# Kernel tuning notes

Hardware: AMD Instinct MI355X
Metric: run time of the kernel (lower is better)

Reference implementation:

```python
import jax, jax.numpy as jnp
import numpy as np

E = 256      # embed_dim
K = 8        # kNN neighbors (hard-coded in module)
B = 64       # num cells (samples)
P = 512      # objects per cell (equal segments)
N = B * P
NUM_CLASSES = 31  # 30 known + <unk> (padding idx 0)


def _normalize(x, axis=-1):
    n = jnp.linalg.norm(x, axis=axis, keepdims=True)
    return x / jnp.clip(n, 1e-12, None)


def _mlp2(x, W1, b1, W2, b2):
    # get_mlp([d_in, 64/E, d_out]): Linear-ReLU-Linear
    return jax.nn.relu(x @ W1 + b1) @ W2 + b2


def setup_inputs() -> dict:
    key = jax.random.key(0)
    ks = jax.random.split(key, 32)

    def w(k, shape, s=0.05):
        return (jax.random.normal(k, shape, jnp.float32) * s).astype(jnp.float32)

    class_table = w(ks[0], (NUM_CLASSES, E))
    class_table = class_table.at[0].set(0.0)  # padding_idx=0

    inp = {
        # learned params
        "class_table": class_table,
        "colorW1": w(ks[1], (3, 64)), "colorb1": jnp.zeros((64,), jnp.float32),
        "colorW2": w(ks[2], (64, E)), "colorb2": jnp.zeros((E,), jnp.float32),
        "posW1": w(ks[3], (3, 64)), "posb1": jnp.zeros((64,), jnp.float32),
        "posW2": w(ks[4], (64, E)), "posb2": jnp.zeros((E,), jnp.float32),
        "mergeW": w(ks[5], (3 * E, E)), "mergeb": jnp.zeros((E,), jnp.float32),
        # DynamicEdgeConv mlp: Linear(2E,E)-ReLU-BN(E)-Linear(E,E)
        "gW1": w(ks[6], (2 * E, E)), "gb1": jnp.zeros((E,), jnp.float32),
        "g_gamma": jnp.ones((E,), jnp.float32), "g_beta": jnp.zeros((E,), jnp.float32),
        "gW2": w(ks[7], (E, E)), "gb2": jnp.zeros((E,), jnp.float32),
        # final lin: Linear(E,E)-ReLU-Linear(E,E)
        "lW1": w(ks[8], (E, E)), "lb1": jnp.zeros((E,), jnp.float32),
        "lW2": w(ks[9], (E, E)), "lb2": jnp.zeros((E,), jnp.float32),
        # forward inputs
        "positions": jax.random.normal(ks[10], (N, 3), jnp.float32),
        "colors": jax.random.uniform(ks[11], (N, 3), jnp.float32),
        "class_indices": jax.random.randint(ks[12], (N,), 0, NUM_CLASSES, jnp.int64),
        "num_samples": B,
    }
    return inp


def reference(class_table, colorW1, colorb1, colorW2, colorb2,
              posW1, posb1, posW2, posb2, mergeW, mergeb,
              gW1, gb1, g_gamma, g_beta, gW2, gb2,
              lW1, lb1, lW2, lb2,
              positions, colors, class_indices, num_samples):
    # --- per-object embeddings, each L2-normalized, then merged ---
    ce = _normalize(class_table[class_indices])                         # [N,E]
    co = _normalize(_mlp2(colors, colorW1, colorb1, colorW2, colorb2))  # [N,E]
    pe = _normalize(_mlp2(positions, posW1, posb1, posW2, posb2))       # [N,E]
    emb = jnp.concatenate([ce, co, pe], axis=-1) @ mergeW + mergeb      # [N,E]

    # --- DynamicEdgeConv (variation 0): per-sample kNN in feature space ---
    x = emb.reshape(num_samples, -1, E)                                 # [B,P,E]
    sq = jnp.sum(x * x, axis=-1)                                        # [B,P]
    dist = sq[:, :, None] + sq[:, None, :] - 2.0 * jnp.einsum('bpe,bqe->bpq', x, x)
    _, idx = jax.lax.top_k(-dist, K)                                    # [B,P,K] (incl. self)

    x_nb = jax.vmap(lambda xb, ib: xb[ib])(x, idx)                      # [B,P,K,E]
    x_i = jnp.broadcast_to(x[:, :, None, :], x_nb.shape)
    msg_in = jnp.concatenate([x_i, x_nb - x_i], axis=-1)                # [B,P,K,2E]
    h = jax.nn.relu(msg_in @ gW1 + gb1)
    h = h * g_gamma + g_beta          # BatchNorm1d eval mode (running mean 0, var 1)
    h = h @ gW2 + gb2                                                   # [B,P,K,E]
    x1 = jnp.max(h, axis=2)                                             # max aggr -> [B,P,E]

    # --- global max pool over objects, final MLP, L2 normalize ---
    pooled = jnp.max(x1, axis=1)                                        # [B,E]
    out = _mlp2(pooled, lW1, lb1, lW2, lb2)
    return _normalize(out, axis=-1)
```

## Files before the change

### kernel.cpp

```cpp
#include <hip/hip_runtime.h>

#define EDIM 256
#define KNN 8
#define NB 64
#define NP 512
#define NTOT (NB * NP)

typedef short s16x8 __attribute__((ext_vector_type(8)));
typedef float f32x4 __attribute__((ext_vector_type(4)));
typedef float f32x16 __attribute__((ext_vector_type(16)));
typedef unsigned short ushort;

__device__ __forceinline__ ushort f2b(float f) {
    unsigned u = __float_as_uint(f);
    u = (u + 0x7fffu + ((u >> 16) & 1u)) >> 16;
    return (ushort)u;
}
__device__ __forceinline__ float b2f(ushort h) {
    return __uint_as_float(((unsigned)h) << 16);
}
__device__ __forceinline__ void split2(float x, ushort& h, ushort& l) {
    h = f2b(x);
    l = f2b(x - b2f(h));
}

__device__ __forceinline__ void gload16(const ushort* g, ushort* l) {
    __builtin_amdgcn_global_load_lds(
        (const __attribute__((address_space(1))) void*)g,
        (__attribute__((address_space(3))) void*)l, 16, 0, 0);
}

__global__ __launch_bounds__(256)
void k_prep(const float* __restrict__ gW1, const float* __restrict__ gW2,
            const float* __restrict__ g_gamma, const float* __restrict__ g_beta,
            const float* __restrict__ gb2,
            const float* __restrict__ cW2, const float* __restrict__ pW2,
            const float* __restrict__ cb2, const float* __restrict__ pb2,
            const float* __restrict__ mW, const float* __restrict__ ct,
            ushort* __restrict__ Wdh, ushort* __restrict__ Wdl,
            ushort* __restrict__ Wbh, ushort* __restrict__ Wbl,
            ushort* __restrict__ g2h, ushort* __restrict__ g2l,
            float* __restrict__ hb,
            ushort* __restrict__ cW2Th, ushort* __restrict__ cW2Tl,
            ushort* __restrict__ pW2Th, ushort* __restrict__ pW2Tl,
            ushort* __restrict__ WcTh, ushort* __restrict__ WcTl,
            ushort* __restrict__ WpTh, ushort* __restrict__ WpTl,
            float* __restrict__ cbM, float* __restrict__ pbM,
            float* __restrict__ classMn)
{
    __shared__ float ctn[256];
    __shared__ float red[4];
    const int bid = blockIdx.x, t = threadIdx.x;
    ushort h, l;

    if (bid < 897) {
        const int gid = bid * 256 + t;
        if (gid < 65536) {
            const int n = gid >> 8, k = gid & 255;
            split2(gW1[k * 256 + n] - gW1[(k + 256) * 256 + n], h, l);
            Wdh[gid] = h; Wdl[gid] = l;
        } else if (gid < 131072) {
            const int i = gid - 65536, n = i >> 8, k = i & 255;
            split2(gW1[(k + 256) * 256 + n], h, l);
            Wbh[i] = h; Wbl[i] = l;
        } else if (gid < 196608) {
            const int i = gid - 131072, n = i >> 8, k = i & 255;
            split2(g_gamma[k] * gW2[k * 256 + n], h, l);
            g2h[i] = h; g2l[i] = l;
        } else if (gid < 196864) {
            const int n = gid - 196608;
            float s = gb2[n];
            for (int k = 0; k < 256; ++k) s += g_beta[k] * gW2[k * 256 + n];
            hb[n] = s;
        } else if (gid < 213248) {
            const int i = gid - 196864, n = i >> 6, k = i & 63;
            split2(cW2[k * 256 + n], h, l);
            cW2Th[i] = h; cW2Tl[i] = l;
        } else if (gid < 229632) {
            const int i = gid - 213248, n = i >> 6, k = i & 63;
            split2(pW2[k * 256 + n], h, l);
            pW2Th[i] = h; pW2Tl[i] = l;
        }
        return;
    }
    if (bid < 1027) {
        const int gid = (bid - 897) * 256 + t;
        if (gid < 16384) {
            const int j = gid >> 8, n = gid & 255;
            float s = 0.f;
            for (int k = 0; k < 256; ++k) s += cW2[j * 256 + k] * mW[(256 + k) * 256 + n];
            split2(s, h, l);
            WcTh[n * 64 + j] = h; WcTl[n * 64 + j] = l;
        } else if (gid < 32768) {
            const int i = gid - 16384, j = i >> 8, n = i & 255;
            float s = 0.f;
            for (int k = 0; k < 256; ++k) s += pW2[j * 256 + k] * mW[(512 + k) * 256 + n];
            split2(s, h, l);
            WpTh[n * 64 + j] = h; WpTl[n * 64 + j] = l;
        } else if (gid < 33024) {
            const int n = gid - 32768;
            float s = 0.f;
            for (int k = 0; k < 256; ++k) s += cb2[k] * mW[(256 + k) * 256 + n];
            cbM[n] = s;
        } else if (gid < 33280) {
            const int n = gid - 33024;
            float s = 0.f;
            for (int k = 0; k < 256; ++k) s += pb2[k] * mW[(512 + k) * 256 + n];
            pbM[n] = s;
        }
        return;
    }
    {
        const int c = bid - 1027;
        const float v = ct[c * 256 + t];
        float ss = v * v;
        #pragma unroll
        for (int s = 32; s > 0; s >>= 1) ss += __shfl_down(ss, s, 64);
        if ((t & 63) == 0) red[t >> 6] = ss;
        __syncthreads();
        const float tot = red[0] + red[1] + red[2] + red[3];
        const float r = 1.f / fmaxf(sqrtf(tot), 1e-12f);
        ctn[t] = v * r;
        __syncthreads();
        float s = 0.f;
        for (int k = 0; k < 256; ++k) s += ctn[k] * mW[k * 256 + t];
        classMn[c * 256 + t] = s;
    }
}

__global__ __launch_bounds__(256)
void k_embed(const float* __restrict__ classMn,
             const float* __restrict__ cW1, const float* __restrict__ cb1,
             const float* __restrict__ cb2,
             const float* __restrict__ pW1, const float* __restrict__ pb1,
             const float* __restrict__ pb2,
             const float* __restrict__ mb,
             const ushort* __restrict__ cW2Th, const ushort* __restrict__ cW2Tl,
             const ushort* __restrict__ pW2Th, const ushort* __restrict__ pW2Tl,
             const ushort* __restrict__ WcTh, const ushort* __restrict__ WcTl,
             const ushort* __restrict__ WpTh, const ushort* __restrict__ WpTl,
             const float* __restrict__ cbM, const float* __restrict__ pbM,
             const float* __restrict__ positions, const float* __restrict__ colors,
             const int* __restrict__ cls, const int cstride,
             ushort* __restrict__ ehi, ushort* __restrict__ elo,
             float* __restrict__ sqn)
{
    __shared__ __align__(16) ushort Ahc[16 * 72];
    __shared__ __align__(16) ushort Alc[16 * 72];
    __shared__ __align__(16) ushort Ahp[16 * 72];
    __shared__ __align__(16) ushort Alp[16 * 72];
    __shared__ float sqc[16][4], sqp_[16][4], sqe[16][4];

    const int t = threadIdx.x, w = t >> 6, lane = t & 63;
    const int l15 = lane & 15, quad = lane >> 4;
    const int obase = blockIdx.x * 16;

    {
        const int o = lane >> 4;
        const int objl = w * 4 + o;
        const int gobj = obase + objl;
        const float c0 = colors[gobj * 3], c1 = colors[gobj * 3 + 1], c2 = colors[gobj * 3 + 2];
        const float q0 = positions[gobj * 3], q1 = positions[gobj * 3 + 1], q2 = positions[gobj * 3 + 2];
        const int u0 = (lane & 15) * 4;
        #pragma unroll
        for (int uu = 0; uu < 4; ++uu) {
            const int u = u0 + uu;
            const float hc = fmaxf(cb1[u] + c0 * cW1[u] + c1 * cW1[64 + u] + c2 * cW1[128 + u], 0.f);
            const float hp = fmaxf(pb1[u] + q0 * pW1[u] + q1 * pW1[64 + u] + q2 * pW1[128 + u], 0.f);
            ushort h, l;
            split2(hc, h, l); Ahc[objl * 72 + u] = h; Alc[objl * 72 + u] = l;
            split2(hp, h, l); Ahp[objl * 72 + u] = h; Alp[objl * 72 + u] = l;
        }
    }
    __syncthreads();

    f32x4 aco[4], ape[4];
    #pragma unroll
    for (int nt = 0; nt < 4; ++nt) { aco[nt] = (f32x4){0.f,0.f,0.f,0.f}; ape[nt] = (f32x4){0.f,0.f,0.f,0.f}; }

    #pragma unroll
    for (int kt = 0; kt < 2; ++kt) {
        const int ao = l15 * 72 + kt * 32 + quad * 8;
        const s16x8 ahc = *(const s16x8*)&Ahc[ao];
        const s16x8 alc = *(const s16x8*)&Alc[ao];
        const s16x8 ahp = *(const s16x8*)&Ahp[ao];
        const s16x8 alp = *(const s16x8*)&Alp[ao];
        #pragma unroll
        for (int nt = 0; nt < 4; ++nt) {
            const int n = w * 64 + nt * 16 + l15;
            const size_t bo = (size_t)n * 64 + kt * 32 + quad * 8;
            const s16x8 cbh = *(const s16x8*)(cW2Th + bo);
            const s16x8 cbl = *(const s16x8*)(cW2Tl + bo);
            const s16x8 pbh = *(const s16x8*)(pW2Th + bo);
            const s16x8 pbl = *(const s16x8*)(pW2Tl + bo);
            aco[nt] = __builtin_amdgcn_mfma_f32_16x16x32_bf16(ahc, cbh, aco[nt], 0, 0, 0);
            ape[nt] = __builtin_amdgcn_mfma_f32_16x16x32_bf16(ahp, pbh, ape[nt], 0, 0, 0);
            aco[nt] = __builtin_amdgcn_mfma_f32_16x16x32_bf16(alc, cbh, aco[nt], 0, 0, 0);
            ape[nt] = __builtin_amdgcn_mfma_f32_16x16x32_bf16(alp, pbh, ape[nt], 0, 0, 0);
            aco[nt] = __builtin_amdgcn_mfma_f32_16x16x32_bf16(ahc, cbl, aco[nt], 0, 0, 0);
            ape[nt] = __builtin_amdgcn_mfma_f32_16x16x32_bf16(ahp, pbl, ape[nt], 0, 0, 0);
        }
    }

    float sc[4] = {0.f,0.f,0.f,0.f}, sp[4] = {0.f,0.f,0.f,0.f};
    #pragma unroll
    for (int nt = 0; nt < 4; ++nt) {
        const int col = w * 64 + nt * 16 + l15;
        const float cbv = cb2[col], pbv = pb2[col];
        #pragma unroll
        for (int r = 0; r < 4; ++r) {
            const float co = aco[nt][r] + cbv;
            const float pe = ape[nt][r] + pbv;
            sc[r] += co * co;
            sp[r] += pe * pe;
        }
    }
    #pragma unroll
    for (int s = 8; s > 0; s >>= 1) {
        #pragma unroll
        for (int r = 0; r < 4; ++r) {
            sc[r] += __shfl_xor(sc[r], s, 64);
            sp[r] += __shfl_xor(sp[r], s, 64);
        }
    }
    if (l15 == 0) {
        #pragma unroll
        for (int r = 0; r < 4; ++r) { sqc[quad * 4 + r][w] = sc[r]; sqp_[quad * 4 + r][w] = sp[r]; }
    }
    __syncthreads();

    float rco[4], rpe[4];
    #pragma unroll
    for (int r = 0; r < 4; ++r) {
        const int row = quad * 4 + r;
        rco[r] = 1.f / fmaxf(sqrtf(sqc[row][0] + sqc[row][1] + sqc[row][2] + sqc[row][3]), 1e-12f);
        rpe[r] = 1.f / fmaxf(sqrtf(sqp_[row][0] + sqp_[row][1] + sqp_[row][2] + sqp_[row][3]), 1e-12f);
    }

    f32x4 ac[4], ap[4];
    #pragma unroll
    for (int nt = 0; nt < 4; ++nt) { ac[nt] = (f32x4){0.f,0.f,0.f,0.f}; ap[nt] = (f32x4){0.f,0.f,0.f,0.f}; }

    #pragma unroll
    for (int kt = 0; kt < 2; ++kt) {
        const int ao = l15 * 72 + kt * 32 + quad * 8;
        const s16x8 ahc = *(const s16x8*)&Ahc[ao];
        const s16x8 alc = *(const s16x8*)&Alc[ao];
        const s16x8 ahp = *(const s16x8*)&Ahp[ao];
        const s16x8 alp = *(const s16x8*)&Alp[ao];
        #pragma unroll
        for (int nt = 0; nt < 4; ++nt) {
            const int n = w * 64 + nt * 16 + l15;
            const size_t bo = (size_t)n * 64 + kt * 32 + quad * 8;
            const s16x8 cbh = *(const s16x8*)(WcTh + bo);
            const s16x8 cbl = *(const s16x8*)(WcTl + bo);
            const s16x8 pbh = *(const s16x8*)(WpTh + bo);
            const s16x8 pbl = *(const s16x8*)(WpTl + bo);
            ac[nt] = __builtin_amdgcn_mfma_f32_16x16x32_bf16(ahc, cbh, ac[nt], 0, 0, 0);
            ap[nt] = __builtin_amdgcn_mfma_f32_16x16x32_bf16(ahp, pbh, ap[nt], 0, 0, 0);
            ac[nt] = __builtin_amdgcn_mfma_f32_16x16x32_bf16(alc, cbh, ac[nt], 0, 0, 0);
            ap[nt] = __builtin_amdgcn_mfma_f32_16x16x32_bf16(alp, pbh, ap[nt], 0, 0, 0);
            ac[nt] = __builtin_amdgcn_mfma_f32_16x16x32_bf16(ahc, cbl, ac[nt], 0, 0, 0);
            ap[nt] = __builtin_amdgcn_mfma_f32_16x16x32_bf16(ahp, pbl, ap[nt], 0, 0, 0);
        }
    }

    int ci[4];
    #pragma unroll
    for (int r = 0; r < 4; ++r) {
        const int gobj = obase + quad * 4 + r;
        int c = cls[(size_t)gobj * cstride];
        if ((unsigned)c > 30u) c = 0;
        ci[r] = c;
    }

    float rp[4] = {0.f,0.f,0.f,0.f};
    #pragma unroll
    for (int nt = 0; nt < 4; ++nt) {
        const int col = w * 64 + nt * 16 + l15;
        const float mbv = mb[col], cbMv = cbM[col], pbMv = pbM[col];
        #pragma unroll
        for (int r = 0; r < 4; ++r) {
            const int row = quad * 4 + r;
            const float e = classMn[ci[r] * 256 + col]
                          + rco[r] * (ac[nt][r] + cbMv)
                          + rpe[r] * (ap[nt][r] + pbMv) + mbv;
            ushort h, l;
            split2(e, h, l);
            ehi[(size_t)(obase + row) * 256 + col] = h;
            elo[(size_t)(obase + row) * 256 + col] = l;
            rp[r] += e * e;
        }
    }
    #pragma unroll
    for (int s = 8; s > 0; s >>= 1) {
        #pragma unroll
        for (int r = 0; r < 4; ++r) rp[r] += __shfl_xor(rp[r], s, 64);
    }
    if (l15 == 0) {
        #pragma unroll
        for (int r = 0; r < 4; ++r) sqe[quad * 4 + r][w] = rp[r];
    }
    __syncthreads();
    if (t < 16) sqn[obase + t] = sqe[t][0] + sqe[t][1] + sqe[t][2] + sqe[t][3];
}

__global__ __launch_bounds__(256)
void k_gram(const ushort* __restrict__ ehi, const ushort* __restrict__ elo,
            const float* __restrict__ sqn, float* __restrict__ dist)
{
    __shared__ __align__(16) ushort lds[2][4][4096];

    const int t = threadIdx.x, w = t >> 6, lane = t & 63;
    const int l15 = lane & 15, quad = lane >> 4;
    const int b = blockIdx.x;
    const int xcd = b & 7, rest = b >> 3;
    const int cell = xcd * 8 + rest / 10;
    const int tt = rest % 10;
    const int ti = (tt < 4) ? 0 : (tt < 7) ? 1 : (tt < 9) ? 2 : 3;
    const int tbase = (ti == 0) ? 0 : (ti == 1) ? 4 : (ti == 2) ? 7 : 9;
    const int tj = ti + (tt - tbase);
    const int p0 = ti * 128, q0 = tj * 128;
    const size_t cb = (size_t)cell * NP;
    const int diag = (ti == tj);
    const int wr = w >> 1, wc = w & 1;

    int srow[2], scol[2];
    #pragma unroll
    for (int i = 0; i < 2; ++i) {
        const int p = (w * 2 + i) * 64 + lane;
        const int row = p >> 2;
        srow[i] = row;
        scol[i] = ((p & 3) ^ ((row >> 1) & 3)) * 8;
    }

    #define STAGE(KT, D)                                                         \
    {                                                                            \
        const int kb_ = (KT) * 32;                                               \
        _Pragma("unroll")                                                        \
        for (int i = 0; i < 2; ++i) {                                            \
            const int ls_ = (w * 2 + i) * 512;               \
            const size_t ga_ = (cb + p0 + srow[i]) * 256 + kb_ + scol[i];        \
            gload16(ehi + ga_, &lds[D][0][ls_]);                                 \
            gload16(elo + ga_, &lds[D][1][ls_]);                                 \
            if (!diag) {                                                         \
                const size_t gq_ = (cb + q0 + srow[i]) * 256 + kb_ + scol[i];    \
                gload16(ehi + gq_, &lds[D][2][ls_]);                             \
                gload16(elo + gq_, &lds[D][3][ls_]);                             \
            }                                                                    \
        }                                                                        \
    }

    f32x4 acc[4][4];
    #pragma unroll
    for (int mt = 0; mt < 4; ++mt)
        #pragma unroll
        for (int nt = 0; nt < 4; ++nt) acc[mt][nt] = (f32x4){0.f, 0.f, 0.f, 0.f};

    const int bB = diag ? 0 : 2;

    STAGE(0, 0);
    __syncthreads();

    for (int kt = 0; kt < 8; ++kt) {
        const int cur = kt & 1;
        if (kt < 7) STAGE(kt + 1, cur ^ 1);

        s16x8 ah[4], al[4];
        #pragma unroll
        for (int mt = 0; mt < 4; ++mt) {
            const int r = wr * 64 + mt * 16 + l15;
            const int slot = 4 * r + (quad ^ ((r >> 1) & 3));
            ah[mt] = *(const s16x8*)&lds[cur][0][slot * 8];
            al[mt] = *(const s16x8*)&lds[cur][1][slot * 8];
        }
        #pragma unroll
        for (int nt = 0; nt < 4; ++nt) {
            const int rq = wc * 64 + nt * 16 + l15;
            const int slot = 4 * rq + (quad ^ ((rq >> 1) & 3));
            const s16x8 bh = *(const s16x8*)&lds[cur][bB][slot * 8];
            const s16x8 bl = *(const s16x8*)&lds[cur][bB + 1][slot * 8];
            #pragma unroll
            for (int mt = 0; mt < 4; ++mt) {
                acc[mt][nt] = __builtin_amdgcn_mfma_f32_16x16x32_bf16(ah[mt], bh, acc[mt][nt], 0, 0, 0);
                acc[mt][nt] = __builtin_amdgcn_mfma_f32_16x16x32_bf16(al[mt], bh, acc[mt][nt], 0, 0, 0);
                acc[mt][nt] = __builtin_amdgcn_mfma_f32_16x16x32_bf16(ah[mt], bl, acc[mt][nt], 0, 0, 0);
            }
        }
        __syncthreads();
    }
    #undef STAGE

    float sqp[4][4];
    #pragma unroll
    for (int mt = 0; mt < 4; ++mt)
        #pragma unroll
        for (int r = 0; r < 4; ++r)
            sqp[mt][r] = sqn[cb + p0 + wr * 64 + mt * 16 + quad * 4 + r];

    float* T = (float*)&lds[0][0][0];

    #pragma unroll
    for (int nt = 0; nt < 4; ++nt) {
        const int cq_l = wc * 64 + nt * 16 + l15;
        const int colq = q0 + cq_l;
        const float sq_q = sqn[cb + colq];
        #pragma unroll
        for (int mt = 0; mt < 4; ++mt) {
            #pragma unroll
            for (int r = 0; r < 4; ++r) {
                const int rp_l = wr * 64 + mt * 16 + quad * 4 + r;
                const float d = (sqp[mt][r] + sq_q) - 2.f * acc[mt][nt][r];
                __builtin_nontemporal_store(d, &dist[(cb + p0 + rp_l) * NP + colq]);
                if (!diag) T[cq_l * 128 + (rp_l ^ ((cq_l & 7) << 4))] = d;
            }
        }
    }

    if (!diag) {
        __syncthreads();
        const int l31 = t & 31, rbase = t >> 5;
        #pragma unroll
        for (int i = 0; i < 16; ++i) {
            const int row = rbase + i * 8;
            const int p4 = l31 * 4;
            const f32x4 vv = *(const f32x4*)&T[row * 128 + (p4 ^ ((row & 7) << 4))];
            __builtin_nontemporal_store(vv, (f32x4*)&dist[(cb + q0 + row) * NP + p0 + p4]);
        }
    }
}

__global__ __launch_bounds__(256)
void k_select(const float* __restrict__ dist, int* __restrict__ nidx)
{
    const int wv = threadIdx.x >> 6, lane = threadIdx.x & 63;
    const int xcd = blockIdx.x & 7, rest = blockIdx.x >> 3;
    const int cell = xcd * 8 + (rest >> 7);
    const int p = cell * NP + (rest & 127) * 4 + wv;
    const float* row = dist + (size_t)p * NP;

    float d[8];
    {
        const float4 va = *(const float4*)(row + lane * 8);
        const float4 vb = *(const float4*)(row + lane * 8 + 4);
        d[0] = va.x; d[1] = va.y; d[2] = va.z; d[3] = va.w;
        d[4] = vb.x; d[5] = vb.y; d[6] = vb.z; d[7] = vb.w;
    }

    for (int r = 0; r < KNN; ++r) {
        float bd = d[0]; int bi = 0;
        #pragma unroll
        for (int i = 1; i < 8; ++i)
            if (d[i] < bd) { bd = d[i]; bi = i; }
        int bq = lane * 8 + bi;
        #pragma unroll
        for (int s = 32; s > 0; s >>= 1) {
            const float od = __shfl_down(bd, s, 64);
            const int oq = __shfl_down(bq, s, 64);
            if (od < bd || (od == bd && oq < bq)) { bd = od; bq = oq; }
        }
        const int win = __shfl(bq, 0, 64);
        if (lane == 0) nidx[(size_t)p * KNN + r] = ((p >> 9) << 9) | win;
        if ((win >> 3) == lane) {
            const int wi = win & 7;
            #pragma unroll
            for (int i = 0; i < 8; ++i) if (wi == i) d[i] = 3.4e38f;
        }
    }
}

__global__ __launch_bounds__(256)
void k_uv(const ushort* __restrict__ ehi, const ushort* __restrict__ elo,
          const ushort* __restrict__ Wdh, const ushort* __restrict__ Wbh,
          const float* __restrict__ gb1,
          float* __restrict__ u, float* __restrict__ v)
{
    (void)elo;
    __shared__ __align__(16) ushort lds[2][2048];

    const int t = threadIdx.x, w = t >> 6, lane = t & 63;
    const int l15 = lane & 15, quad = lane >> 4;
    const int isV = blockIdx.x >> 9;
    const int m0 = (blockIdx.x & 511) * 64;
    const ushort* Wh = isV ? Wbh : Wdh;
    float* out = isV ? v : u;
    const int mh = w & 1, ch = w >> 1;

    const int sp = w * 64 + lane;
    const int srow = sp >> 2;
    const int scol = ((sp & 3) ^ ((srow >> 1) & 3)) * 8;

    #define STAGE_UV(S, D)                                                       \
    {                                                                            \
        const size_t ga_ = (size_t)(m0 + srow) * 256 + (S) * 32 + scol;          \
        gload16(ehi + ga_, &lds[D][sp * 8]);                                     \
    }

    const int r0 = mh * 32 + l15, r1 = r0 + 16;
    const int slot0 = 4 * r0 + (quad ^ ((r0 >> 1) & 3));
    const int slot1 = 4 * r1 + (quad ^ ((r1 >> 1) & 3));

    f32x4 acc[2][8];
    #pragma unroll
    for (int mt = 0; mt < 2; ++mt)
        #pragma unroll
        for (int nt = 0; nt < 8; ++nt) acc[mt][nt] = (f32x4){0.f, 0.f, 0.f, 0.f};

    STAGE_UV(0, 0);
    __syncthreads();

    for (int s = 0; s < 8; ++s) {
        const int cur = s & 1;
        if (s < 7) STAGE_UV(s + 1, cur ^ 1);

        const s16x8 ah0 = *(const s16x8*)&lds[cur][slot0 * 8];
        const s16x8 ah1 = *(const s16x8*)&lds[cur][slot1 * 8];
        #pragma unroll
        for (int nt = 0; nt < 8; ++nt) {
            const int n = ch * 128 + nt * 16 + l15;
            const size_t bo = (size_t)n * 256 + s * 32 + quad * 8;
            const s16x8 bh = *(const s16x8*)(Wh + bo);
            acc[0][nt] = __builtin_amdgcn_mfma_f32_16x16x32_bf16(ah0, bh, acc[0][nt], 0, 0, 0);
            acc[1][nt] = __builtin_amdgcn_mfma_f32_16x16x32_bf16(ah1, bh, acc[1][nt], 0, 0, 0);
        }
        __syncthreads();
    }
    #undef STAGE_UV

    #pragma unroll
    for (int mt = 0; mt < 2; ++mt) {
        #pragma unroll
        for (int nt = 0; nt < 8; ++nt) {
            const int col = ch * 128 + nt * 16 + l15;
            const float bias = isV ? 0.f : gb1[col];
            #pragma unroll
            for (int r = 0; r < 4; ++r) {
                const int row = mh * 32 + mt * 16 + quad * 4 + r;
                out[(size_t)(m0 + row) * 256 + col] = acc[mt][nt][r] + bias;
            }
        }
    }
}

__global__ __launch_bounds__(512)
void k_edge(const float* __restrict__ u, const float* __restrict__ v,
            const int* __restrict__ nidx,
            const ushort* __restrict__ g2h,
            const float* __restrict__ hb,
            float* __restrict__ part)
{
    __shared__ ushort Abuf[2][2304];
    __shared__ float ustage[2048];

    const int t = threadIdx.x, w = t >> 6, lane = t & 63;
    const int l31 = lane & 31, kh = lane >> 5;

    const int b = blockIdx.x;
    const int xcd = b & 7, rest = b >> 3;
    const int cell = xcd * 8 + (rest >> 6);
    const int pl0 = cell * NP + (rest & 63) * 8;

    {
        const int pt = t >> 6, kk = (t & 63) * 4;
        *(float4*)&ustage[pt * 256 + kk] = *(const float4*)(u + (size_t)(pl0 + pt) * 256 + kk);
    }

    const int se = t >> 3, kq = t & 7;
    const int upt = se >> 3;
    int svrow = nidx[(size_t)(pl0 + upt) * KNN + (se & 7)];
    if ((unsigned)svrow >= (unsigned)NTOT) svrow = 0;

    __syncthreads();

    float4 vr[2];

    #define VLOAD(S)                                                             \
    {                                                                            \
        const int k0 = (S) * 32 + kq * 4;                                        \
        vr[(S) & 1] = *(const float4*)(v + (size_t)svrow * 256 + k0);            \
    }
    #define SPLITW(S, BUF)                                                       \
    {                                                                            \
        const int k0u = (S) * 32 + kq * 4;                                       \
        const float4 ua = *(const float4*)&ustage[upt * 256 + k0u];              \
        const float4 va = vr[(S) & 1];                                           \
        const float sv[4] = {                                                    \
            fmaxf(ua.x + va.x, 0.f), fmaxf(ua.y + va.y, 0.f),                    \
            fmaxf(ua.z + va.z, 0.f), fmaxf(ua.w + va.w, 0.f)};                   \
        union { uint2 q; ushort us[4]; } th;                                     \
        _Pragma("unroll")                                                        \
        for (int j = 0; j < 4; ++j) { th.us[j] = f2b(sv[j]); }                   \
        *(uint2*)&Abuf[BUF][se * 36 + kq * 4] = th.q;                            \
    }

    #define LDS_BARRIER()                                                        \
    {                                                                            \
        asm volatile("s_waitcnt lgkmcnt(0)" ::: "memory");                       \
        __builtin_amdgcn_s_barrier();                                            \
    }

    f32x16 acc[2];
    acc[0] = (f32x16)(0.0f);
    acc[1] = (f32x16)(0.0f);

    VLOAD(0); VLOAD(1);
    SPLITW(0, 0);

    #pragma unroll
    for (int s = 0; s < 8; ++s) {
        LDS_BARRIER();
        if (s < 7) {
            SPLITW(s + 1, (s + 1) & 1);
            if (s < 6) VLOAD(s + 2);
        }

        s16x8 ah[2][2];
        #pragma unroll
        for (int mt = 0; mt < 2; ++mt) {
            #pragma unroll
            for (int kc = 0; kc < 2; ++kc) {
                const int ao = (mt * 32 + l31) * 36 + kc * 16 + kh * 8;
                union { uint2 q[2]; s16x8 v8; } Th;
                Th.q[0] = *(const uint2*)&Abuf[s & 1][ao];
                Th.q[1] = *(const uint2*)&Abuf[s & 1][ao + 4];
                ah[mt][kc] = Th.v8;
            }
        }

        #pragma unroll
        for (int kc = 0; kc < 2; ++kc) {
            const int n = w * 32 + l31;
            const s16x8 bh = *(const s16x8*)(g2h + (size_t)n * 256 + s * 32 + kc * 16 + kh * 8);
            acc[0] = __builtin_amdgcn_mfma_f32_32x32x16_bf16(ah[0][kc], bh, acc[0], 0, 0, 0);
            acc[1] = __builtin_amdgcn_mfma_f32_32x32x16_bf16(ah[1][kc], bh, acc[1], 0, 0, 0);
        }
    }
    #undef VLOAD
    #undef SPLITW
    #undef LDS_BARRIER

    const int slot = rest & 63;
    {
        float rm = -3.4e38f;
        #pragma unroll
        for (int r = 0; r < 16; ++r)
            rm = fmaxf(rm, fmaxf(acc[0][r], acc[1][r]));
        rm = fmaxf(rm, __shfl_xor(rm, 32, 64));
        if (kh == 0) {
            const int col = w * 32 + l31;
            part[((size_t)cell * 64 + slot) * 256 + col] = rm + hb[col];
        }
    }
}

__global__ __launch_bounds__(256)
void k_final(const float* __restrict__ part,
             const float* __restrict__ lW1, const float* __restrict__ lb1,
             const float* __restrict__ lW2, const float* __restrict__ lb2,
             float* __restrict__ out)
{
    __shared__ float pooled[256];
    __shared__ float hid[256];
    __shared__ float red[4];

    const int b = blockIdx.x;
    const int t = threadIdx.x;

    float m = -3.4e38f;
    for (int s = 0; s < 64; ++s)
        m = fmaxf(m, part[((size_t)b * 64 + s) * 256 + t]);
    pooled[t] = m;
    __syncthreads();

    float h = lb1[t];
    for (int k = 0; k < 256; k += 4) {
        #pragma unroll
        for (int kk = 0; kk < 4; ++kk)
            h += pooled[k + kk] * lW1[(k + kk) * 256 + t];
    }
    hid[t] = fmaxf(h, 0.f);
    __syncthreads();

    float o = lb2[t];
    for (int k = 0; k < 256; k += 4) {
        #pragma unroll
        for (int kk = 0; kk < 4; ++kk)
            o += hid[k + kk] * lW2[(k + kk) * 256 + t];
    }

    float ss = o * o;
    #pragma unroll
    for (int s = 32; s > 0; s >>= 1) ss += __shfl_down(ss, s, 64);
    if ((t & 63) == 0) red[t >> 6] = ss;
    __syncthreads();
    const float tot = red[0] + red[1] + red[2] + red[3];
    const float rn = 1.f / fmaxf(sqrtf(tot), 1e-12f);
    out[b * 256 + t] = o * rn;
}

extern "C" void kernel_launch(void* const* d_in, const int* in_sizes, int n_in,
                              void* d_out, int out_size, void* d_ws, size_t ws_size,
                              hipStream_t stream)
{
    (void)n_in; (void)out_size; (void)ws_size;

    const float* class_table = (const float*)d_in[0];
    const float* cW1 = (const float*)d_in[1];
    const float* cb1 = (const float*)d_in[2];
    const float* cW2 = (const float*)d_in[3];
    const float* cb2 = (const float*)d_in[4];
    const float* pW1 = (const float*)d_in[5];
    const float* pb1 = (const float*)d_in[6];
    const float* pW2 = (const float*)d_in[7];
    const float* pb2 = (const float*)d_in[8];
    const float* mW  = (const float*)d_in[9];
    const float* mb  = (const float*)d_in[10];
    const float* gW1 = (const float*)d_in[11];
    const float* gb1 = (const float*)d_in[12];
    const float* g_gamma = (const float*)d_in[13];
    const float* g_beta  = (const float*)d_in[14];
    const float* gW2 = (const float*)d_in[15];
    const float* gb2 = (const float*)d_in[16];
    const float* lW1 = (const float*)d_in[17];
    const float* lb1 = (const float*)d_in[18];
    const float* lW2 = (const float*)d_in[19];
    const float* lb2 = (const float*)d_in[20];
    const float* positions = (const float*)d_in[21];
    const float* colors    = (const float*)d_in[22];
    const int*  cls        = (const int*)d_in[23];

    const int cstride = (in_sizes[23] == 2 * NTOT) ? 2 : 1;

    char* base = (char*)d_ws;
    float*   part   = (float*)(base + 0);
    ushort*  Wdh    = (ushort*)(base + 4194304);
    ushort*  Wdl    = (ushort*)(base + 4325376);
    ushort*  Wbh    = (ushort*)(base + 4456448);
    ushort*  Wbl    = (ushort*)(base + 4587520);
    ushort*  g2h    = (ushort*)(base + 4718592);
    ushort*  g2l    = (ushort*)(base + 4849664);
    float*   hb     = (float*)(base + 4980736);
    ushort*  cW2Th  = (ushort*)(base + 4981760);
    ushort*  cW2Tl  = (ushort*)(base + 5014528);
    ushort*  pW2Th  = (ushort*)(base + 5047296);
    ushort*  pW2Tl  = (ushort*)(base + 5080064);
    ushort*  WcTh   = (ushort*)(base + 5112832);
    ushort*  WcTl   = (ushort*)(base + 5145600);
    ushort*  WpTh   = (ushort*)(base + 5178368);
    ushort*  WpTl   = (ushort*)(base + 5211136);
    float*   classMn= (float*)(base + 5243904);
    float*   cbM    = (float*)(base + 5275648);
    float*   pbM    = (float*)(base + 5276672);
    int*     nidx   = (int*)(base + 5277696);
    float*   sqn    = (float*)(base + 6326272);
    ushort*  ehi    = (ushort*)(base + 6457344);
    ushort*  elo    = (ushort*)(base + 23234560);
    float*   dist   = (float*)(base + 40011776);
    float*   v      = (float*)(base + 107120640);
    float*   u      = (float*)(base + 140675072);
    float* out = (float*)d_out;

    k_prep<<<1058, 256, 0, stream>>>(gW1, gW2, g_gamma, g_beta, gb2, cW2, pW2,
                                     cb2, pb2, mW, class_table,
                                     Wdh, Wdl, Wbh, Wbl, g2h, g2l, hb,
                                     cW2Th, cW2Tl, pW2Th, pW2Tl,
                                     WcTh, WcTl, WpTh, WpTl, cbM, pbM, classMn);

    k_embed<<<NTOT / 16, 256, 0, stream>>>(classMn, cW1, cb1, cb2, pW1, pb1, pb2,
                                           mb, cW2Th, cW2Tl, pW2Th, pW2Tl,
                                           WcTh, WcTl, WpTh, WpTl, cbM, pbM,
                                           positions, colors, cls, cstride,
                                           ehi, elo, sqn);
    k_gram<<<NB * 10, 256, 0, stream>>>(ehi, elo, sqn, dist);
    k_select<<<NTOT / 4, 256, 0, stream>>>(dist, nidx);
    k_uv<<<2 * NTOT / 64, 256, 0, stream>>>(ehi, elo, Wdh, Wbh, gb1, u, v);
    k_edge<<<NTOT / 8, 512, 0, stream>>>(u, v, nidx, g2h, hb, part);
    k_final<<<NB, 256, 0, stream>>>(part, lW1, lb1, lW2, lb2, out);
}
```

Before: 404.9 us.

## Fuse per-tile top-8 selection into gram kernel, replace full distance matrix with candidates

The gram kernel no longer writes the full 512x512 fp32 distance matrix per cell. Each 128x128 tile now computes a partial top-8 per row (and per column for off-diagonal tiles) from LDS, using packed 64-bit key/index insertion sorts. A small k_nidx kernel merges the 4 per-tile candidate lists per point into the final 8 neighbors. This removes roughly 67MB of distance writes and reads plus the wave-wide shuffle selection, but adds serial insertion-sort work inside the gram epilogue, with only two threads per row.

```diff
diff --git a/kernel.cpp b/kernel.cpp
--- a/kernel.cpp
+++ b/kernel.cpp
@@ -10,6 +10,7 @@
 typedef float f32x4 __attribute__((ext_vector_type(4)));
 typedef float f32x16 __attribute__((ext_vector_type(16)));
 typedef unsigned short ushort;
+typedef unsigned long long u64;
 
 __device__ __forceinline__ ushort f2b(float f) {
     unsigned u = __float_as_uint(f);
@@ -22,6 +23,18 @@
 __device__ __forceinline__ void split2(float x, ushort& h, ushort& l) {
     h = f2b(x);
     l = f2b(x - b2f(h));
+}
+
+__device__ __forceinline__ unsigned fkey(float f) {
+    const unsigned b = __float_as_uint(f);
+    return (b & 0x80000000u) ? ~b : (b | 0x80000000u);
+}
+
+__device__ __forceinline__ void ins8(u64* k, u64 x) {
+    #pragma unroll
+    for (int j = 7; j >= 1; --j)
+        k[j] = (x < k[j - 1]) ? k[j - 1] : ((x < k[j]) ? x : k[j]);
+    k[0] = (x < k[0]) ? x : k[0];
 }
 
 __device__ __forceinline__ void gload16(const ushort* g, ushort* l) {
@@ -307,7 +320,7 @@
 
 __global__ __launch_bounds__(256)
 void k_gram(const ushort* __restrict__ ehi, const ushort* __restrict__ elo,
-            const float* __restrict__ sqn, float* __restrict__ dist)
+            const float* __restrict__ sqn, u64* __restrict__ cand)
 {
     __shared__ __align__(16) ushort lds[2][4][4096];
 
@@ -403,70 +416,82 @@
     #pragma unroll
     for (int nt = 0; nt < 4; ++nt) {
         const int cq_l = wc * 64 + nt * 16 + l15;
-        const int colq = q0 + cq_l;
-        const float sq_q = sqn[cb + colq];
+        const float sq_q = sqn[cb + q0 + cq_l];
         #pragma unroll
         for (int mt = 0; mt < 4; ++mt) {
             #pragma unroll
             for (int r = 0; r < 4; ++r) {
                 const int rp_l = wr * 64 + mt * 16 + quad * 4 + r;
                 const float d = (sqp[mt][r] + sq_q) - 2.f * acc[mt][nt][r];
-                __builtin_nontemporal_store(d, &dist[(cb + p0 + rp_l) * NP + colq]);
-                if (!diag) T[cq_l * 128 + (rp_l ^ ((cq_l & 7) << 4))] = d;
+                T[rp_l * 128 + (cq_l ^ rp_l)] = d;
             }
         }
     }
-
-    if (!diag) {
-        __syncthreads();
-        const int l31 = t & 31, rbase = t >> 5;
-        #pragma unroll
-        for (int i = 0; i < 16; ++i) {
-            const int row = rbase + i * 8;
-            const int p4 = l31 * 4;
-            const f32x4 vv = *(const f32x4*)&T[row * 128 + (p4 ^ ((row & 7) << 4))];
-            __builtin_nontemporal_store(vv, (f32x4*)&dist[(cb + q0 + row) * NP + p0 + p4]);
+    __syncthreads();
+
+    {
+        const int row = t >> 1, half = t & 1;
+
+        u64 k8[8];
+        #pragma unroll
+        for (int j = 0; j < 8; ++j) k8[j] = ~0ull;
+        for (int c = 0; c < 64; ++c) {
+            const int cc = half * 64 + c;
+            const float f = T[row * 128 + (cc ^ row)];
+            ins8(k8, ((u64)fkey(f) << 32) | (unsigned)(q0 + cc));
+        }
+        {
+            u64 part[8];
+            #pragma unroll
+            for (int j = 0; j < 8; ++j) part[j] = __shfl_xor(k8[j], 1, 64);
+            #pragma unroll
+            for (int j = 0; j < 8; ++j) ins8(k8, part[j]);
+        }
+        if (half == 0) {
+            u64* cp = cand + ((size_t)(cb + p0 + row)) * 32 + tj * 8;
+            #pragma unroll
+            for (int j = 0; j < 8; ++j) cp[j] = k8[j];
+        }
+
+        if (!diag) {
+            u64 q8[8];
+            #pragma unroll
+            for (int j = 0; j < 8; ++j) q8[j] = ~0ull;
+            for (int c = 0; c < 64; ++c) {
+                const int rr = half * 64 + c;
+                const float f = T[rr * 128 + (row ^ rr)];
+                ins8(q8, ((u64)fkey(f) << 32) | (unsigned)(p0 + rr));
+            }
+            {
+                u64 part[8];
+                #pragma unroll
+                for (int j = 0; j < 8; ++j) part[j] = __shfl_xor(q8[j], 1, 64);
+                #pragma unroll
+                for (int j = 0; j < 8; ++j) ins8(q8, part[j]);
+            }
+            if (half == 0) {
+                u64* cp = cand + ((size_t)(cb + q0 + row)) * 32 + ti * 8;
+                #pragma unroll
+                for (int j = 0; j < 8; ++j) cp[j] = q8[j];
+            }
         }
     }
 }
 
 __global__ __launch_bounds__(256)
-void k_select(const float* __restrict__ dist, int* __restrict__ nidx)
+void k_nidx(const u64* __restrict__ cand, int* __restrict__ nidx)
 {
-    const int wv = threadIdx.x >> 6, lane = threadIdx.x & 63;
-    const int xcd = blockIdx.x & 7, rest = blockIdx.x >> 3;
-    const int cell = xcd * 8 + (rest >> 7);
-    const int p = cell * NP + (rest & 127) * 4 + wv;
-    const float* row = dist + (size_t)p * NP;
-
-    float d[8];
-    {
-        const float4 va = *(const float4*)(row + lane * 8);
-        const float4 vb = *(const float4*)(row + lane * 8 + 4);
-        d[0] = va.x; d[1] = va.y; d[2] = va.z; d[3] = va.w;
-        d[4] = vb.x; d[5] = vb.y; d[6] = vb.z; d[7] = vb.w;
-    }
-
-    for (int r = 0; r < KNN; ++r) {
-        float bd = d[0]; int bi = 0;
-        #pragma unroll
-        for (int i = 1; i < 8; ++i)
-            if (d[i] < bd) { bd = d[i]; bi = i; }
-        int bq = lane * 8 + bi;
-        #pragma unroll
-        for (int s = 32; s > 0; s >>= 1) {
-            const float od = __shfl_down(bd, s, 64);
-            const int oq = __shfl_down(bq, s, 64);
-            if (od < bd || (od == bd && oq < bq)) { bd = od; bq = oq; }
-        }
-        const int win = __shfl(bq, 0, 64);
-        if (lane == 0) nidx[(size_t)p * KNN + r] = ((p >> 9) << 9) | win;
-        if ((win >> 3) == lane) {
-            const int wi = win & 7;
-            #pragma unroll
-            for (int i = 0; i < 8; ++i) if (wi == i) d[i] = 3.4e38f;
-        }
-    }
+    const int p = blockIdx.x * 256 + threadIdx.x;
+    const u64* cp = cand + (size_t)p * 32;
+    u64 k8[8];
+    #pragma unroll
+    for (int j = 0; j < 8; ++j) k8[j] = ~0ull;
+    #pragma unroll
+    for (int i = 0; i < 32; ++i) ins8(k8, cp[i]);
+    const int hi = (p >> 9) << 9;
+    #pragma unroll
+    for (int r = 0; r < 8; ++r)
+        nidx[(size_t)p * KNN + r] = hi | (int)(k8[r] & 0x1ffu);
 }
 
 __global__ __launch_bounds__(256)
@@ -755,7 +780,7 @@
     float*   sqn    = (float*)(base + 6326272);
     ushort*  ehi    = (ushort*)(base + 6457344);
     ushort*  elo    = (ushort*)(base + 23234560);
-    float*   dist   = (float*)(base + 40011776);
+    u64*     cand   = (u64*)(base + 40011776);
     float*   v      = (float*)(base + 107120640);
     float*   u      = (float*)(base + 140675072);
     float* out = (float*)d_out;
@@ -771,8 +796,8 @@
                                            WcTh, WcTl, WpTh, WpTl, cbM, pbM,
                                            positions, colors, cls, cstride,
                                            ehi, elo, sqn);
-    k_gram<<<NB * 10, 256, 0, stream>>>(ehi, elo, sqn, dist);
-    k_select<<<NTOT / 4, 256, 0, stream>>>(dist, nidx);
+    k_gram<<<NB * 10, 256, 0, stream>>>(ehi, elo, sqn, cand);
+    k_nidx<<<NTOT / 256, 256, 0, stream>>>(cand, nidx);
     k_uv<<<2 * NTOT / 64, 256, 0, stream>>>(ehi, elo, Wdh, Wbh, gb1, u, v);
     k_edge<<<NTOT / 8, 512, 0, stream>>>(u, v, nidx, g2h, hb, part);
     k_final<<<NB, 256, 0, stream>>>(part, lW1, lb1, lW2, lb2, out);
```

Result: no change. 404.0 us (-0.2%).
